# Kernel tuning notes

Measured on AMD Instinct MI355X. Metric: run time of the kernel, lower is better.

The kernel has to match this reference:

```python
import jax, jax.numpy as jnp
import numpy as np

NUM_HEADS = 16


def _window_for_epoch(epoch: int) -> int:
    # Faithful reproduction of the module's (buggy) branch structure:
    # epoch<5 sets mask_4, elif epoch<10 sets mask_6, but then an
    # independent `if epoch < 15` overwrites with mask_8, else mask_10.
    if epoch < 15:
        return 16  # mask_8 -> w=16
    return 20      # mask_10 -> w=20


def setup_inputs() -> dict:
    key = jax.random.key(0)
    ks = jax.random.split(key, 4)
    B, N, C = 2, 2048, 1024
    x = jax.random.normal(ks[0], (B, N, C), dtype=jnp.float32)
    qkv_w = jax.random.normal(ks[1], (3 * C, C), dtype=jnp.float32) * (C ** -0.5)
    proj_w = jax.random.normal(ks[2], (C, C), dtype=jnp.float32) * (C ** -0.5)
    proj_b = jnp.zeros((C,), dtype=jnp.float32)
    return {"x": x, "qkv_w": qkv_w, "proj_w": proj_w, "proj_b": proj_b, "epoch": 0}


def reference(x, qkv_w, proj_w, proj_b, epoch):
    B, N, C = x.shape
    H = NUM_HEADS
    Dh = C // H
    scale = float(Dh // H)  # head_dim // num_heads (integer division), =4

    qkv = jnp.einsum('bnc,dc->bnd', x, qkv_w)           # [B,N,3C]
    qkv = qkv.reshape(B, N, 3, H, Dh).transpose(2, 0, 3, 1, 4)
    q, k, v = qkv[0], qkv[1], qkv[2]                    # each [B,H,N,Dh]

    attn = jnp.einsum('bhnd,bhmd->bhnm', q, k) * scale  # [B,H,N,N]

    w = _window_for_epoch(int(epoch))
    idx = jnp.arange(N)
    band = jnp.abs(idx[:, None] - idx[None, :]) <= w    # [N,N] sliding window
    # Original fills masked logits with 1e-9 (NOT -inf) before softmax.
    attn = jnp.where(band[None, None], attn, jnp.float32(1e-9))
    attn = jax.nn.softmax(attn, axis=-1)

    out = jnp.einsum('bhnm,bhmd->bhnd', attn, v)        # [B,H,N,Dh]
    out = out.transpose(0, 2, 1, 3).reshape(B, N, C)
    out = jnp.einsum('bnc,dc->bnd', out, proj_w) + proj_b
    return out
```

## Files before the change

### kernel.cpp

```cpp
#include <hip/hip_runtime.h>
#include <cstddef>


typedef _Float16 f16x8 __attribute__((ext_vector_type(8)));
typedef float    f32x4 __attribute__((ext_vector_type(4)));

#define MFMA16(a, b, c) __builtin_amdgcn_mfma_f32_16x16x32_f16((a), (b), (c), 0, 0, 0)

__device__ __forceinline__ void gl_lds16(const void* g, void* l) {
    __builtin_amdgcn_global_load_lds(
        (const __attribute__((address_space(1))) void*)g,
        (__attribute__((address_space(3))) void*)l, 16, 0, 0);
}

__device__ __forceinline__ ushort f2h(float f) {
    _Float16 h = (_Float16)f;
    return *(ushort*)&h;
}

__global__ void split_all(const float* __restrict__ x,
                          const float* __restrict__ qkvw,
                          const float* __restrict__ projw,
                          ushort* __restrict__ x16,
                          ushort* __restrict__ w16,
                          ushort* __restrict__ pw16,
                          float* __restrict__ sall)
{
    const int i = blockIdx.x * 256 + threadIdx.x;
    if (i < 512) ((float4*)sall)[i] = make_float4(0.f, 0.f, 0.f, 0.f);
    const float* src; ushort* dst; int j;
    if (i < 1048576)      { src = x;     dst = x16;  j = i; }
    else if (i < 1835008) { src = qkvw;  dst = w16;  j = i - 1048576; }
    else                  { src = projw; dst = pw16; j = i - 1835008; }

    float4 v = ((const float4*)src)[j];
    ((ushort4*)dst)[j] = make_ushort4(f2h(v.x), f2h(v.y), f2h(v.z), f2h(v.w));
}

__global__ __launch_bounds__(512, 2) void gemm_qkv_pipe(
    const ushort* __restrict__ A_g, const ushort* __restrict__ W_g,
    ushort* __restrict__ out16, float* __restrict__ sall)
{
    const int K = 1024;
    __shared__ ushort sm[73728];

    const int tid  = threadIdx.x;
    const int wid  = tid >> 6;
    const int lane = tid & 63;
    const int quad = lane >> 4;
    const int cl   = lane & 15;

    const int bsw = (blockIdx.x & 7) * 32 + (blockIdx.x >> 3);
    const int m0 = (bsw >> 4) * 256;
    const int n0 = (bsw & 15) * 192;

    const int wr = wid >> 2;
    const int wc = wid & 3;

    const int lrow = lane >> 2;
    const int sl   = lane & 3;
    const int rA1 = wid * 16 + lrow;
    const int rA2 = 128 + rA1;
    const int rB1 = wid * 16 + lrow;
    const int rB2 = 128 + (wid & 3) * 16 + lrow;

    const ushort* sA1 = A_g + (size_t)(m0 + rA1) * K + ((sl ^ ((rA1 >> 1) & 3)) * 8);
    const ushort* sA2 = A_g + (size_t)(m0 + rA2) * K + ((sl ^ ((rA2 >> 1) & 3)) * 8);
    const ushort* sB1 = W_g + (size_t)(n0 + rB1) * K + ((sl ^ ((rB1 >> 1) & 3)) * 8);
    const ushort* sB2 = W_g + (size_t)(n0 + rB2) * K + ((sl ^ ((rB2 >> 1) & 3)) * 8);

    const int dA1 = wid * 512;
    const int dA2 = 4096 + wid * 512;
    const int dB1 = 8192 + wid * 512;

    int aoff[8], boff[3];
#pragma unroll
    for (int mg = 0; mg < 8; ++mg) {
        const int row = wr * 128 + mg * 16 + cl;
        aoff[mg] = row * 32 + ((quad ^ ((row >> 1) & 3)) * 8);
    }
#pragma unroll
    for (int ng = 0; ng < 3; ++ng) {
        const int row = wc * 48 + ng * 16 + cl;
        boff[ng] = 8192 + row * 32 + ((quad ^ ((row >> 1) & 3)) * 8);
    }

    f32x4 acc[8][3];
#pragma unroll
    for (int mg = 0; mg < 8; ++mg)
#pragma unroll
        for (int ng = 0; ng < 3; ++ng) acc[mg][ng] = (f32x4){0.f, 0.f, 0.f, 0.f};

    int kst = 0;

#define STAGE_T(BUF) do {                                                    \
    const int bo_ = (BUF) * 14336;                                           \
    gl_lds16(sA1 + kst, sm + bo_ + dA1);                                     \
    gl_lds16(sA2 + kst, sm + bo_ + dA2);                                     \
    gl_lds16(sB1 + kst, sm + bo_ + dB1);                                     \
    ushort* pB2_ = (wid < 4) ? (sm + bo_ + 12288 + wid * 512)                \
                             : (sm + 71680 + (wid & 3) * 512);               \
    gl_lds16(sB2 + kst, pB2_);                                               \
    kst += 32;                                                               \
} while (0)

#define COMPUTE_T(BUF) do {                                                  \
    const int co_ = (BUF) * 14336;                                           \
    f16x8 af[8]; f16x8 bf[3];                                                \
    _Pragma("unroll")                                                        \
    for (int mg = 0; mg < 8; ++mg) af[mg] = *(const f16x8*)&sm[co_ + aoff[mg]]; \
    _Pragma("unroll")                                                        \
    for (int ng = 0; ng < 3; ++ng) bf[ng] = *(const f16x8*)&sm[co_ + boff[ng]]; \
    __builtin_amdgcn_s_setprio(1);                                           \
    _Pragma("unroll")                                                        \
    for (int mg = 0; mg < 8; ++mg)                                           \
        _Pragma("unroll")                                                    \
        for (int ng = 0; ng < 3; ++ng)                                       \
            acc[mg][ng] = MFMA16(af[mg], bf[ng], acc[mg][ng]);               \
    __builtin_amdgcn_s_setprio(0);                                           \
} while (0)

#define WAITBAR(N) do {                                                      \
    asm volatile("s_waitcnt vmcnt(" #N ")" ::: "memory");                    \
    __builtin_amdgcn_s_barrier();                                            \
    asm volatile("" ::: "memory");                                           \
} while (0)

    STAGE_T(0); STAGE_T(1); STAGE_T(2); STAGE_T(3);

    int bc = 0, bs = 4;
    for (int t = 0; t < 28; ++t) {
        WAITBAR(12);
        STAGE_T(bs);
        COMPUTE_T(bc);
        bc = (bc == 4) ? 0 : bc + 1;
        bs = (bs == 4) ? 0 : bs + 1;
    }
    WAITBAR(12); COMPUTE_T(bc); bc = (bc == 4) ? 0 : bc + 1;
    WAITBAR(8);  COMPUTE_T(bc); bc = (bc == 4) ? 0 : bc + 1;
    WAITBAR(4);  COMPUTE_T(bc); bc = (bc == 4) ? 0 : bc + 1;
    WAITBAR(0);  COMPUTE_T(bc);

#undef STAGE_T
#undef COMPUTE_T
#undef WAITBAR

#pragma unroll
    for (int mg = 0; mg < 8; ++mg)
#pragma unroll
        for (int r = 0; r < 4; ++r) {
            const int gm = m0 + wr * 128 + mg * 16 + quad * 4 + r;
            const int bq = gm >> 11;
            const int nn = gm & 2047;
#pragma unroll
            for (int ng = 0; ng < 3; ++ng) {
                const int gn = n0 + wc * 48 + ng * 16 + cl;
                const int sq = gn >> 10;
                const int h  = (gn >> 6) & 15;
                const int dh = gn & 63;
                out16[(size_t)sq * 4194304u + (((size_t)bq * 16 + h) * 2048 + nn) * 64 + dh]
                    = f2h(acc[mg][ng][r]);
            }
        }

    const int bq2 = (m0 + wr * 128) >> 11;
#pragma unroll
    for (int ng = 0; ng < 3; ++ng) {
        const int gbase = n0 + wc * 48 + ng * 16;
        if (gbase >= 2048) {
            float ps = 0.f;
#pragma unroll
            for (int mg = 0; mg < 8; ++mg)
#pragma unroll
                for (int r = 0; r < 4; ++r) ps += acc[mg][ng][r];
            ps += __shfl_xor(ps, 16);
            ps += __shfl_xor(ps, 32);
            if (quad == 0) {
                const int h = (gbase >> 6) & 15;
                atomicAdd(&sall[(bq2 * 16 + h) * 64 + (gbase & 63) + cl], ps);
            }
        }
    }
}

__global__ __launch_bounds__(256, 2) void gemm_proj(
    const ushort* __restrict__ A_g, const ushort* __restrict__ W_g,
    const float* __restrict__ bias, float* __restrict__ out)
{
    const int K = 1024, Nout = 1024;
    __shared__ ushort smem[24576];

    const int tid  = threadIdx.x;
    const int wid  = tid >> 6;
    const int lane = tid & 63;
    const int quad = lane >> 4;
    const int cl   = lane & 15;
    const int m0 = blockIdx.y * 64;
    const int n0 = blockIdx.x * 128;
    const int wm = (wid & 1) * 32;
    const int wn = (wid >> 1) * 64;

    const int srow = lane >> 2;
    const int scol = (lane & 3) * 8;

    f32x4 acc[2][4];
#pragma unroll
    for (int i = 0; i < 2; ++i)
#pragma unroll
        for (int j = 0; j < 4; ++j) acc[i][j] = (f32x4){0.f, 0.f, 0.f, 0.f};

    for (int k0 = 0; k0 < K; k0 += 128) {
#pragma unroll
        for (int c = 0; c < 12; ++c) {
            const int cid = wid * 12 + c;
            const ushort* s; ushort* d; int rr, pl;
            if (cid < 16) {
                pl = cid >> 2;
                const int ch = cid & 3;
                s = A_g; rr = m0 + ch * 16;
                d = smem + pl * 2048 + ch * 512;
            } else {
                const int wcx = cid - 16;
                pl = wcx >> 3;
                const int ch = wcx & 7;
                s = W_g; rr = n0 + ch * 16;
                d = smem + 8192 + pl * 4096 + ch * 512;
            }
            gl_lds16(s + (size_t)(rr + srow) * K + k0 + pl * 32 + scol, d);
        }
        __syncthreads();

#pragma unroll
        for (int pl = 0; pl < 4; ++pl) {
            const ushort* ASp = smem + pl * 2048;
            const ushort* WSp = smem + 8192 + pl * 4096;
            f16x8 a[2], w[4];
#pragma unroll
            for (int i = 0; i < 2; ++i)
                a[i] = ((const f16x8*)ASp)[(wm + i * 16 + cl) * 4 + quad];
#pragma unroll
            for (int i = 0; i < 4; ++i)
                w[i] = ((const f16x8*)WSp)[(wn + i * 16 + cl) * 4 + quad];
#pragma unroll
            for (int mi = 0; mi < 2; ++mi)
#pragma unroll
                for (int ni = 0; ni < 4; ++ni)
                    acc[mi][ni] = MFMA16(a[mi], w[ni], acc[mi][ni]);
        }
        __syncthreads();
    }

    float bb[4];
#pragma unroll
    for (int ni = 0; ni < 4; ++ni) bb[ni] = bias[n0 + wn + ni * 16 + cl];
#pragma unroll
    for (int mi = 0; mi < 2; ++mi)
#pragma unroll
        for (int r = 0; r < 4; ++r) {
            const int gm = m0 + wm + mi * 16 + quad * 4 + r;
            float* rowp = out + (size_t)gm * Nout;
#pragma unroll
            for (int ni = 0; ni < 4; ++ni) {
                const int gn = n0 + wn + ni * 16 + cl;
                rowp[gn] = acc[mi][ni][r] + bb[ni];
            }
        }
}

__global__ __launch_bounds__(512) void attn_mfma(
    const ushort* __restrict__ qg, const ushort* __restrict__ kg,
    const ushort* __restrict__ vg,
    const float* __restrict__ sall,
    ushort* __restrict__ outp,
    const int* __restrict__ epoch_ptr)
{
    const int N = 2048;
    const int w = (epoch_ptr[0] < 15) ? 16 : 20;

    __shared__ ushort Pl[8][16][72];
    __shared__ ushort VT[64][180];

    const int tid  = threadIdx.x;
    const int wid  = tid >> 6;
    const int lane = tid & 63;
    const int quad = lane >> 4;
    const int cl   = lane & 15;

    const int bh = blockIdx.x >> 4;
    const int n0 = (blockIdx.x & 15) << 7;
    const int lo = max(0, n0 - w);
    const int wm = wid << 4;
    const int hi = min(N - 1, n0 + 127 + w);
    const int cnt = hi - lo + 1;

    for (int t = tid; t < 64 * 26; t += 512) {
        const int row = t / 26;
        const int c2  = 128 + (t - row * 26) * 2;
        *(unsigned*)&VT[row][c2] = 0u;
    }
    __syncthreads();

    for (int t = tid; t < 168 * 8; t += 512) {
        const int s  = t >> 3;
        const int db = (t & 7) * 8;
        if (s < cnt) {
            uint4 vv = *(const uint4*)(vg + (((size_t)bh * N) + lo + s) * 64 + db);
            VT[db + 0][s] = (ushort)(vv.x & 0xffff); VT[db + 1][s] = (ushort)(vv.x >> 16);
            VT[db + 2][s] = (ushort)(vv.y & 0xffff); VT[db + 3][s] = (ushort)(vv.y >> 16);
            VT[db + 4][s] = (ushort)(vv.z & 0xffff); VT[db + 5][s] = (ushort)(vv.z >> 16);
            VT[db + 6][s] = (ushort)(vv.w & 0xffff); VT[db + 7][s] = (ushort)(vv.w >> 16);
        }
    }

    const int jminw = max(0, n0 + wm - w);
    const int sbase = ((jminw - lo) >> 3) << 3;

    const ushort* qp = qg + ((size_t)bh * N + n0 + wm + cl) * 64;
    const f16x8 aq0 = *(const f16x8*)(qp + quad * 8);
    const f16x8 aq1 = *(const f16x8*)(qp + 32 + quad * 8);

    f32x4 sacc[4];
#pragma unroll
    for (int ni = 0; ni < 4; ++ni) {
        int krow = lo + sbase + ni * 16 + cl;
        krow = min(krow, N - 1);
        const ushort* kp = kg + ((size_t)bh * N + krow) * 64;
        const f16x8 bk0 = *(const f16x8*)(kp + quad * 8);
        const f16x8 bk1 = *(const f16x8*)(kp + 32 + quad * 8);
        f32x4 s = (f32x4){0.f, 0.f, 0.f, 0.f};
        s = MFMA16(aq0, bk0, s);
        s = MFMA16(aq1, bk1, s);
        sacc[ni] = s;
    }
#pragma unroll
    for (int ni = 0; ni < 4; ++ni) sacc[ni] *= 4.0f;

    float pm[4];
#pragma unroll
    for (int r = 0; r < 4; ++r) {
        const int n = n0 + wm + quad * 4 + r;
        const int jlo = max(0, n - w), jhi = min(N - 1, n + w);
        const int bc = jhi - jlo + 1;
        float mx = 1e-9f;
#pragma unroll
        for (int ni = 0; ni < 4; ++ni) {
            const int j = lo + sbase + ni * 16 + cl;
            const bool val = (j >= n - w) && (j <= n + w) && (j < N);
            const float sv = sacc[ni][r];
            if (val) mx = fmaxf(mx, sv);
        }
        mx = fmaxf(mx, __shfl_xor(mx, 1));
        mx = fmaxf(mx, __shfl_xor(mx, 2));
        mx = fmaxf(mx, __shfl_xor(mx, 4));
        mx = fmaxf(mx, __shfl_xor(mx, 8));
        const float em = __expf(1e-9f - mx);
        float e[4];
        float sum = 0.f;
#pragma unroll
        for (int ni = 0; ni < 4; ++ni) {
            const int j = lo + sbase + ni * 16 + cl;
            const bool val = (j >= n - w) && (j <= n + w) && (j < N);
            const float ev = val ? __expf(sacc[ni][r] - mx) : 0.f;
            e[ni] = val ? (ev - em) : 0.f;
            sum += ev;
        }
        sum += __shfl_xor(sum, 1);
        sum += __shfl_xor(sum, 2);
        sum += __shfl_xor(sum, 4);
        sum += __shfl_xor(sum, 8);
        const float inv = __builtin_amdgcn_rcpf((float)(N - bc) * em + sum);
        pm[r] = em * inv;
#pragma unroll
        for (int ni = 0; ni < 4; ++ni)
            sacc[ni][r] = e[ni] * inv;
    }

#pragma unroll
    for (int ni = 0; ni < 4; ++ni)
#pragma unroll
        for (int r = 0; r < 4; ++r)
            Pl[wid][quad * 4 + r][ni * 16 + cl] = f2h(sacc[ni][r]);

    __syncthreads();

    const int b = bh >> 4, h = bh & 15;
#pragma unroll
    for (int dn = 0; dn < 4; ++dn) {
        f32x4 o = (f32x4){0.f, 0.f, 0.f, 0.f};
#pragma unroll
        for (int k0 = 0; k0 < 64; k0 += 32) {
            const f16x8 a  = *(const f16x8*)&Pl[wid][cl][k0 + quad * 8];
            const f16x8 bb = *(const f16x8*)&VT[dn * 16 + cl][sbase + k0 + quad * 8];
            o = MFMA16(a, bb, o);
        }
        const int d = dn * 16 + cl;
        const float sv = sall[bh * 64 + d];
#pragma unroll
        for (int r = 0; r < 4; ++r) {
            const int n = n0 + wm + quad * 4 + r;
            outp[((size_t)b * N + n) * 1024 + h * 64 + d] = f2h(o[r] + pm[r] * sv);
        }
    }
}

extern "C" void kernel_launch(void* const* d_in, const int* in_sizes, int n_in,
                              void* d_out, int out_size, void* d_ws, size_t ws_size,
                              hipStream_t stream)
{
    const float* x      = (const float*)d_in[0];
    const float* qkv_w  = (const float*)d_in[1];
    const float* proj_w = (const float*)d_in[2];
    const float* proj_b = (const float*)d_in[3];
    const int*   epoch  = (const int*)d_in[4];
    float* out = (float*)d_out;

    const size_t BHND = (size_t)2 * 16 * 2048 * 64;
    const size_t XN = 4194304, WN = 3145728;

    ushort* qkv16 = (ushort*)d_ws;
    ushort* q16   = qkv16;
    ushort* k16   = qkv16 + BHND;
    ushort* v16   = qkv16 + 2 * BHND;
    float*  sall  = (float*)(qkv16 + 3 * BHND);
    ushort* x16   = (ushort*)(sall + 4096);
    ushort* w16   = x16 + XN;
    ushort* pw16  = w16 + WN;
    ushort* ao    = x16;

    split_all<<<dim3(8192), dim3(256), 0, stream>>>(
        x, qkv_w, proj_w, x16, w16, pw16, sall);

    gemm_qkv_pipe<<<dim3(256), dim3(512), 0, stream>>>(x16, w16, qkv16, sall);

    attn_mfma<<<dim3(512), dim3(512), 0, stream>>>(q16, k16, v16, sall, ao, epoch);

    gemm_proj<<<dim3(8, 64), dim3(256), 0, stream>>>(ao, pw16, proj_b, out);
}
```

Baseline: 145.3 us.

## Rewrite projection GEMM with multi-stage async LDS pipeline and larger tiles

```diff
diff --git a/kernel.cpp b/kernel.cpp
--- a/kernel.cpp
+++ b/kernel.cpp
@@ -143,7 +143,6 @@
 
 #undef STAGE_T
 #undef COMPUTE_T
-#undef WAITBAR
 
 #pragma unroll
     for (int mg = 0; mg < 8; ++mg)
@@ -181,88 +180,127 @@
             }
         }
     }
-}
-
-__global__ __launch_bounds__(256, 2) void gemm_proj(
+#undef WAITBAR
+}
+
+__global__ __launch_bounds__(256, 2) void gemm_proj_pipe(
     const ushort* __restrict__ A_g, const ushort* __restrict__ W_g,
     const float* __restrict__ bias, float* __restrict__ out)
 {
     const int K = 1024, Nout = 1024;
-    __shared__ ushort smem[24576];
+    __shared__ ushort sm[40960];
 
     const int tid  = threadIdx.x;
     const int wid  = tid >> 6;
     const int lane = tid & 63;
     const int quad = lane >> 4;
     const int cl   = lane & 15;
-    const int m0 = blockIdx.y * 64;
-    const int n0 = blockIdx.x * 128;
-    const int wm = (wid & 1) * 32;
+
+    const int bsw = (blockIdx.x & 7) * 32 + (blockIdx.x >> 3);
+    const int m0 = (bsw >> 3) * 128;
+    const int n0 = (bsw & 7) * 128;
+
+    const int wm = (wid & 1) * 64;
     const int wn = (wid >> 1) * 64;
 
-    const int srow = lane >> 2;
-    const int scol = (lane & 3) * 8;
-
-    f32x4 acc[2][4];
-#pragma unroll
-    for (int i = 0; i < 2; ++i)
-#pragma unroll
-        for (int j = 0; j < 4; ++j) acc[i][j] = (f32x4){0.f, 0.f, 0.f, 0.f};
-
-    for (int k0 = 0; k0 < K; k0 += 128) {
-#pragma unroll
-        for (int c = 0; c < 12; ++c) {
-            const int cid = wid * 12 + c;
-            const ushort* s; ushort* d; int rr, pl;
-            if (cid < 16) {
-                pl = cid >> 2;
-                const int ch = cid & 3;
-                s = A_g; rr = m0 + ch * 16;
-                d = smem + pl * 2048 + ch * 512;
-            } else {
-                const int wcx = cid - 16;
-                pl = wcx >> 3;
-                const int ch = wcx & 7;
-                s = W_g; rr = n0 + ch * 16;
-                d = smem + 8192 + pl * 4096 + ch * 512;
-            }
-            gl_lds16(s + (size_t)(rr + srow) * K + k0 + pl * 32 + scol, d);
-        }
-        __syncthreads();
-
-#pragma unroll
-        for (int pl = 0; pl < 4; ++pl) {
-            const ushort* ASp = smem + pl * 2048;
-            const ushort* WSp = smem + 8192 + pl * 4096;
-            f16x8 a[2], w[4];
-#pragma unroll
-            for (int i = 0; i < 2; ++i)
-                a[i] = ((const f16x8*)ASp)[(wm + i * 16 + cl) * 4 + quad];
-#pragma unroll
-            for (int i = 0; i < 4; ++i)
-                w[i] = ((const f16x8*)WSp)[(wn + i * 16 + cl) * 4 + quad];
-#pragma unroll
-            for (int mi = 0; mi < 2; ++mi)
-#pragma unroll
-                for (int ni = 0; ni < 4; ++ni)
-                    acc[mi][ni] = MFMA16(a[mi], w[ni], acc[mi][ni]);
-        }
-        __syncthreads();
-    }
+    const int lrow = lane >> 2;
+    const int sl   = lane & 3;
+    const int r1 = wid * 16 + lrow;
+    const int r2 = 64 + r1;
+
+    const ushort* sA1 = A_g + (size_t)(m0 + r1) * K + ((sl ^ ((r1 >> 1) & 3)) * 8);
+    const ushort* sA2 = A_g + (size_t)(m0 + r2) * K + ((sl ^ ((r2 >> 1) & 3)) * 8);
+    const ushort* sB1 = W_g + (size_t)(n0 + r1) * K + ((sl ^ ((r1 >> 1) & 3)) * 8);
+    const ushort* sB2 = W_g + (size_t)(n0 + r2) * K + ((sl ^ ((r2 >> 1) & 3)) * 8);
+
+    const int dA1 = wid * 512;
+    const int dA2 = 2048 + wid * 512;
+    const int dB1 = 4096 + wid * 512;
+    const int dB2 = 6144 + wid * 512;
+
+    int aoff[4], boff[4];
+#pragma unroll
+    for (int mg = 0; mg < 4; ++mg) {
+        const int row = wm + mg * 16 + cl;
+        aoff[mg] = row * 32 + ((quad ^ ((row >> 1) & 3)) * 8);
+    }
+#pragma unroll
+    for (int ng = 0; ng < 4; ++ng) {
+        const int row = wn + ng * 16 + cl;
+        boff[ng] = 4096 + row * 32 + ((quad ^ ((row >> 1) & 3)) * 8);
+    }
+
+    f32x4 acc[4][4];
+#pragma unroll
+    for (int mg = 0; mg < 4; ++mg)
+#pragma unroll
+        for (int ng = 0; ng < 4; ++ng) acc[mg][ng] = (f32x4){0.f, 0.f, 0.f, 0.f};
+
+    int kst = 0;
+
+#define STAGE_P(BUF) do {                                                    \
+    const int bo_ = (BUF) * 8192;                                            \
+    gl_lds16(sA1 + kst, sm + bo_ + dA1);                                     \
+    gl_lds16(sA2 + kst, sm + bo_ + dA2);                                     \
+    gl_lds16(sB1 + kst, sm + bo_ + dB1);                                     \
+    gl_lds16(sB2 + kst, sm + bo_ + dB2);                                     \
+    kst += 32;                                                               \
+} while (0)
+
+#define COMPUTE_P(BUF) do {                                                  \
+    const int co_ = (BUF) * 8192;                                            \
+    f16x8 af[4]; f16x8 bf[4];                                                \
+    _Pragma("unroll")                                                        \
+    for (int mg = 0; mg < 4; ++mg) af[mg] = *(const f16x8*)&sm[co_ + aoff[mg]]; \
+    _Pragma("unroll")                                                        \
+    for (int ng = 0; ng < 4; ++ng) bf[ng] = *(const f16x8*)&sm[co_ + boff[ng]]; \
+    __builtin_amdgcn_s_setprio(1);                                           \
+    _Pragma("unroll")                                                        \
+    for (int mg = 0; mg < 4; ++mg)                                           \
+        _Pragma("unroll")                                                    \
+        for (int ng = 0; ng < 4; ++ng)                                       \
+            acc[mg][ng] = MFMA16(af[mg], bf[ng], acc[mg][ng]);               \
+    __builtin_amdgcn_s_setprio(0);                                           \
+} while (0)
+
+#define WAITBAR(N) do {                                                      \
+    asm volatile("s_waitcnt vmcnt(" #N ")" ::: "memory");                    \
+    __builtin_amdgcn_s_barrier();                                            \
+    asm volatile("" ::: "memory");                                           \
+} while (0)
+
+    STAGE_P(0); STAGE_P(1); STAGE_P(2); STAGE_P(3);
+
+    int bc = 0, bs = 4;
+    for (int t = 0; t < 28; ++t) {
+        WAITBAR(12);
+        STAGE_P(bs);
+        COMPUTE_P(bc);
+        bc = (bc == 4) ? 0 : bc + 1;
+        bs = (bs == 4) ? 0 : bs + 1;
+    }
+    WAITBAR(12); COMPUTE_P(bc); bc = (bc == 4) ? 0 : bc + 1;
+    WAITBAR(8);  COMPUTE_P(bc); bc = (bc == 4) ? 0 : bc + 1;
+    WAITBAR(4);  COMPUTE_P(bc); bc = (bc == 4) ? 0 : bc + 1;
+    WAITBAR(0);  COMPUTE_P(bc);
+
+#undef STAGE_P
+#undef COMPUTE_P
+#undef WAITBAR
 
     float bb[4];
 #pragma unroll
-    for (int ni = 0; ni < 4; ++ni) bb[ni] = bias[n0 + wn + ni * 16 + cl];
-#pragma unroll
-    for (int mi = 0; mi < 2; ++mi)
+    for (int ng = 0; ng < 4; ++ng) bb[ng] = bias[n0 + wn + ng * 16 + cl];
+#pragma unroll
+    for (int mg = 0; mg < 4; ++mg)
 #pragma unroll
         for (int r = 0; r < 4; ++r) {
-            const int gm = m0 + wm + mi * 16 + quad * 4 + r;
+            const int gm = m0 + wm + mg * 16 + quad * 4 + r;
             float* rowp = out + (size_t)gm * Nout;
 #pragma unroll
-            for (int ni = 0; ni < 4; ++ni) {
-                const int gn = n0 + wn + ni * 16 + cl;
-                rowp[gn] = acc[mi][ni][r] + bb[ni];
+            for (int ng = 0; ng < 4; ++ng) {
+                const int gn = n0 + wn + ng * 16 + cl;
+                rowp[gn] = acc[mg][ng][r] + bb[ng];
             }
         }
 }
@@ -434,5 +472,5 @@
 
     attn_mfma<<<dim3(512), dim3(512), 0, stream>>>(q16, k16, v16, sall, ao, epoch);
 
-    gemm_proj<<<dim3(8, 64), dim3(256), 0, stream>>>(ao, pw16, proj_b, out);
-}
+    gemm_proj_pipe<<<dim3(256), dim3(256), 0, stream>>>(ao, pw16, proj_b, out);
+}
```

Result: no change. 143.1 us (-1.5%).
